# Kernel tuning notes

Measured on AMD Instinct MI355X. Metric: run time of the kernel, lower is better.

The kernel has to match this reference:

```python
import jax, jax.numpy as jnp
import numpy as np

B, S, D = 1, 2048, 1024
HEADS, HEAD_DIM = 16, 64
GRID = (8, 16, 16)      # frames, height, width; prod == S
WIN = (3, 5, 5)         # window_f, window_h, window_w
NEG = -1e9


def _window_mask_3d(frames, height, width, wf, wh, ww):
    """[S, S] bool mask: True where kv is inside the 3D local window of q."""
    idx = np.arange(frames * height * width)
    f = idx // (height * width)
    hw = idx % (height * width)
    h = hw // width
    w = hw % width
    mf = np.abs(f[:, None] - f[None, :]) <= wf // 2
    mh = np.abs(h[:, None] - h[None, :]) <= wh // 2
    mw = np.abs(w[:, None] - w[None, :]) <= ww // 2
    return jnp.asarray(mf & mh & mw)


def setup_inputs() -> dict:
    key = jax.random.key(0)
    ks = jax.random.split(key, 6)
    sd = 1.0 / np.sqrt(D)
    return {
        "hidden_states": jax.random.normal(ks[0], (B, S, D), jnp.float32),
        "Wq": jax.random.normal(ks[1], (D, D), jnp.float32) * sd,
        "Wk": jax.random.normal(ks[2], (D, D), jnp.float32) * sd,
        "Wv": jax.random.normal(ks[3], (D, D), jnp.float32) * sd,
        "Wo": jax.random.normal(ks[4], (D, D), jnp.float32) * sd,
        "bo": jnp.zeros((D,), jnp.float32),
        "frames": GRID[0], "height": GRID[1], "width": GRID[2],
        "wf": WIN[0], "wh": WIN[1], "ww": WIN[2],
    }


def reference(hidden_states, Wq, Wk, Wv, Wo, bo, frames, height, width, wf, wh, ww):
    b, s, d = hidden_states.shape
    hd = d // HEADS
    scale = 1.0 / np.sqrt(hd)

    # QKV projections (attn.to_q / to_k / to_v, bias=False), self-attention
    q = (hidden_states @ Wq).reshape(b, s, HEADS, hd).transpose(0, 2, 1, 3)
    k = (hidden_states @ Wk).reshape(b, s, HEADS, hd).transpose(0, 2, 1, 3)
    v = (hidden_states @ Wv).reshape(b, s, HEADS, hd).transpose(0, 2, 1, 3)

    mask = _window_mask_3d(frames, height, width, wf, wh, ww)  # [S, S] bool

    # SDPA with boolean attn_mask (window-based block-sparse pattern)
    scores = jnp.einsum("bhqd,bhkd->bhqk", q, k) * scale
    scores = jnp.where(mask[None, None], scores, NEG)
    attnw = jax.nn.softmax(scores, axis=-1)
    out = jnp.einsum("bhqk,bhkd->bhqd", attnw, v)

    out = out.transpose(0, 2, 1, 3).reshape(b, s, d)
    return out @ Wo + bo
```

## Files before the change

### kernel.cpp

```cpp
#include <hip/hip_runtime.h>
#include <hip/hip_bf16.h>
#include <hip/hip_fp16.h>

#define SEQ   2048
#define DIM   1024
#define NHEAD 16
#define HD    64
#define QSCALE 0.18033688011112042f

typedef _Float16 half8 __attribute__((ext_vector_type(8)));
typedef _Float16 half4 __attribute__((ext_vector_type(4)));
typedef float    floatx4 __attribute__((ext_vector_type(4)));

__device__ __forceinline__ void gload16(const void* g, void* l) {
    __builtin_amdgcn_global_load_lds(
        (const __attribute__((address_space(1))) unsigned int*)g,
        (__attribute__((address_space(3))) unsigned int*)l, 16, 0, 0);
}

#define VMCNT(n) asm volatile("s_waitcnt vmcnt(" #n ")" ::: "memory")
#define LGKM0()  asm volatile("s_waitcnt lgkmcnt(0)" ::: "memory")
#define BAR()    __builtin_amdgcn_s_barrier()

__global__ __launch_bounds__(256) void prep(
        const float* __restrict__ H, _Float16* __restrict__ Hf,
        const float* __restrict__ W0, const float* __restrict__ W1,
        const float* __restrict__ W2, const float* __restrict__ W3,
        _Float16* __restrict__ T) {
    __shared__ float tile[64][65];
    int z = blockIdx.z;
    int t = threadIdx.x;
    if (z < 4) {
        const float* W = (z == 0) ? W0 : (z == 1) ? W1 : (z == 2) ? W2 : W3;
        _Float16* Tz = T + (size_t)z * (DIM * DIM);
        int bx = blockIdx.x * 64;
        int by = blockIdx.y * 64;
        #pragma unroll
        for (int i = 0; i < 4; i++) {
            int id = t + i * 256;
            int r = id >> 4;
            int c = (id & 15) * 4;
            float4 v = *reinterpret_cast<const float4*>(W + (size_t)(by + r) * DIM + bx + c);
            tile[r][c] = v.x; tile[r][c + 1] = v.y; tile[r][c + 2] = v.z; tile[r][c + 3] = v.w;
        }
        __syncthreads();
        #pragma unroll
        for (int i = 0; i < 2; i++) {
            int id = t + i * 256;
            int nr = id >> 3;
            int c8 = id & 7;
            half8 o;
            #pragma unroll
            for (int j = 0; j < 8; j++) o[j] = (_Float16)tile[c8 * 8 + j][nr];
            *reinterpret_cast<half8*>(Tz + (size_t)(bx + nr) * DIM + by + c8 * 8) = o;
        }
    } else {
        int wg = blockIdx.y * 16 + blockIdx.x;
        #pragma unroll
        for (int i = 0; i < 4; i++) {
            int base = ((wg * 4 + i) * 256 + t) * 8;
            float4 v0 = *reinterpret_cast<const float4*>(H + base);
            float4 v1 = *reinterpret_cast<const float4*>(H + base + 4);
            half8 o = { (_Float16)v0.x, (_Float16)v0.y, (_Float16)v0.z, (_Float16)v0.w,
                        (_Float16)v1.x, (_Float16)v1.y, (_Float16)v1.z, (_Float16)v1.w };
            *reinterpret_cast<half8*>(Hf + base) = o;
        }
    }
}

__device__ __forceinline__ void gemm_core(const _Float16* __restrict__ Ap,
                                          const _Float16* __restrict__ Bp,
                                          char* lds, floatx4 (&acc)[4][4]) {
    const int tid  = threadIdx.x;
    const int lane = tid & 63;
    const int wid  = tid >> 6;
    const int wr = wid >> 1, wc = wid & 1;
    const int r16 = lane & 15;
    const int kk  = (lane >> 4) * 8;

    const int srow = tid >> 2, scol = (tid & 3) * 8;
    const _Float16* As0 = Ap + (size_t)srow * DIM + scol;
    const _Float16* Bs0 = Bp + (size_t)srow * DIM + scol;

    auto stage = [&](int buf, int t) {
        char* Ad = lds + buf * 32768;
        char* Bd = Ad + 16384;
        int k0 = t * 64;
        #pragma unroll
        for (int i = 0; i < 4; i++) {
            int off = (i & 1) * 64 * DIM + (i >> 1) * 32 + k0;
            gload16(As0 + off, Ad + i * 4096 + wid * 1024);
            gload16(Bs0 + off, Bd + i * 4096 + wid * 1024);
        }
    };

    auto compute = [&](int buf) {
        char* Ad = lds + buf * 32768;
        char* Bd = Ad + 16384;
        #pragma unroll
        for (int ks = 0; ks < 2; ks++) {
            half8 a[4], b[4];
            #pragma unroll
            for (int m = 0; m < 4; m++)
                a[m] = *reinterpret_cast<half8*>(Ad + ks * 8192 + (wr * 64 + m * 16 + r16) * 64 + kk * 2);
            #pragma unroll
            for (int n = 0; n < 4; n++)
                b[n] = *reinterpret_cast<half8*>(Bd + ks * 8192 + (wc * 64 + n * 16 + r16) * 64 + kk * 2);
            #pragma unroll
            for (int m = 0; m < 4; m++)
                #pragma unroll
                for (int n = 0; n < 4; n++)
                    acc[m][n] = __builtin_amdgcn_mfma_f32_16x16x32_f16(a[m], b[n], acc[m][n], 0, 0, 0);
        }
    };

    stage(0, 0);
    stage(1, 1);
    #pragma unroll 1
    for (int t = 0; t < 14; t += 2) {
        VMCNT(8); BAR();
        compute(0);
        BAR();
        stage(0, t + 2);
        VMCNT(8); BAR();
        compute(1);
        BAR();
        stage(1, t + 3);
    }
    VMCNT(8); BAR();
    compute(0);
    BAR();
    VMCNT(0); BAR();
    compute(1);
}

__device__ __forceinline__ void gemm_core64(const _Float16* __restrict__ Ap,
                                            const _Float16* __restrict__ Bp,
                                            char* lds, floatx4 (&acc)[4][2]) {
    const int tid  = threadIdx.x;
    const int lane = tid & 63;
    const int wid  = tid >> 6;
    const int wr = wid >> 1, wc = wid & 1;
    const int r16 = lane & 15;
    const int kk  = (lane >> 4) * 8;

    const int srow = tid >> 2, scol = (tid & 3) * 8;
    const _Float16* As0 = Ap + (size_t)srow * DIM + scol;
    const _Float16* Bs0 = Bp + (size_t)srow * DIM + scol;

    auto stage = [&](int buf, int t) {
        char* Ad = lds + buf * 24576;
        char* Bd = Ad + 16384;
        int k0 = t * 64;
        #pragma unroll
        for (int i = 0; i < 4; i++) {
            int off = (i & 1) * 64 * DIM + (i >> 1) * 32 + k0;
            gload16(As0 + off, Ad + i * 4096 + wid * 1024);
        }
        #pragma unroll
        for (int j = 0; j < 2; j++)
            gload16(Bs0 + j * 32 + k0, Bd + j * 4096 + wid * 1024);
    };

    auto compute = [&](int buf) {
        char* Ad = lds + buf * 24576;
        char* Bd = Ad + 16384;
        #pragma unroll
        for (int ks = 0; ks < 2; ks++) {
            half8 a[4], b[2];
            #pragma unroll
            for (int m = 0; m < 4; m++)
                a[m] = *reinterpret_cast<half8*>(Ad + ks * 8192 + (wr * 64 + m * 16 + r16) * 64 + kk * 2);
            #pragma unroll
            for (int n = 0; n < 2; n++)
                b[n] = *reinterpret_cast<half8*>(Bd + ks * 4096 + (wc * 32 + n * 16 + r16) * 64 + kk * 2);
            #pragma unroll
            for (int m = 0; m < 4; m++)
                #pragma unroll
                for (int n = 0; n < 2; n++)
                    acc[m][n] = __builtin_amdgcn_mfma_f32_16x16x32_f16(a[m], b[n], acc[m][n], 0, 0, 0);
        }
    };

    stage(0, 0);
    stage(1, 1);
    #pragma unroll 1
    for (int t = 0; t < 14; t += 2) {
        VMCNT(6); BAR();
        compute(0);
        BAR();
        stage(0, t + 2);
        VMCNT(6); BAR();
        compute(1);
        BAR();
        stage(1, t + 3);
    }
    VMCNT(6); BAR();
    compute(0);
    BAR();
    VMCNT(0); BAR();
    compute(1);
}

__global__ __launch_bounds__(256) void gemm_qkv(
        const _Float16* __restrict__ Hf, const _Float16* __restrict__ Wt,
        _Float16* __restrict__ Qp, _Float16* __restrict__ Kp, _Float16* __restrict__ Vt) {
    __shared__ char lds[65536];
    floatx4 acc[4][4] = {};

    int lin = blockIdx.x + 16 * blockIdx.y + 128 * blockIdx.z;
    int swz = (lin & 7) * 48 + (lin >> 3);
    int z  = swz >> 7;
    int rem = swz & 127;
    int bx = rem & 15, by = rem >> 4;

    int tm, tn;
    const _Float16 *Ap, *Bp;
    if (z < 2) {
        tm = bx; tn = by;
        Ap = Hf + (size_t)tm * 128 * DIM;
        Bp = Wt + (size_t)z * DIM * DIM + (size_t)tn * 128 * DIM;
    } else {
        tm = bx & 7; tn = by * 2 + (bx >> 3);
        Ap = Wt + (size_t)2 * DIM * DIM + (size_t)tm * 128 * DIM;
        Bp = Hf + (size_t)tn * 128 * DIM;
    }
    gemm_core(Ap, Bp, lds, acc);

    int lane = threadIdx.x & 63, wid = threadIdx.x >> 6;
    int wr = wid >> 1, wc = wid & 1;
    float qs = (z == 0) ? QSCALE : 1.0f;
    _Float16* Oz = (z == 0) ? Qp : Kp;

    #pragma unroll
    for (int m = 0; m < 4; m++) {
        #pragma unroll
        for (int n = 0; n < 4; n++) {
            #pragma unroll
            for (int r = 0; r < 4; r++) {
                int row = tm * 128 + wr * 64 + m * 16 + (lane >> 4) * 4 + r;
                int col = tn * 128 + wc * 64 + n * 16 + (lane & 15);
                float v = acc[m][n][r];
                if (z < 2) {
                    int head = col >> 6;
                    Oz[(size_t)head * (SEQ * HD) + (size_t)row * HD + (col & 63)] = (_Float16)(v * qs);
                } else {
                    Vt[(size_t)row * SEQ + col] = (_Float16)v;
                }
            }
        }
    }
}

__global__ __launch_bounds__(256) void gemm_o(
        const _Float16* __restrict__ AO, const _Float16* __restrict__ WoT,
        const float* __restrict__ bias, float* __restrict__ out) {
    __shared__ char lds[49152];
    floatx4 acc[4][2] = {};

    int lin = blockIdx.x + 16 * blockIdx.y;
    int swz = (lin & 7) * 32 + (lin >> 3);
    int tm = swz & 15, tn = swz >> 4;

    gemm_core64(AO + (size_t)tm * 128 * DIM, WoT + (size_t)tn * 64 * DIM, lds, acc);

    int lane = threadIdx.x & 63, wid = threadIdx.x >> 6;
    int wr = wid >> 1, wc = wid & 1;
    #pragma unroll
    for (int m = 0; m < 4; m++) {
        #pragma unroll
        for (int n = 0; n < 2; n++) {
            #pragma unroll
            for (int r = 0; r < 4; r++) {
                int row = tm * 128 + wr * 64 + m * 16 + (lane >> 4) * 4 + r;
                int col = tn * 64 + wc * 32 + n * 16 + (lane & 15);
                out[(size_t)row * DIM + col] = acc[m][n][r] + bias[col];
            }
        }
    }
}

__global__ __launch_bounds__(256) void attn_mfma(
        const _Float16* __restrict__ Q,
        const _Float16* __restrict__ K,
        const _Float16* __restrict__ Vt,
        _Float16* __restrict__ AO) {
    __shared__ char P_lds[4][16 * 640];

    int wid  = threadIdx.x >> 6;
    int lane = threadIdx.x & 63;
    int g    = lane >> 4;
    int ql   = lane & 15;

    int blk  = blockIdx.x;
    int sblk = (blk & 7) * 64 + (blk >> 3);
    int bid  = sblk * 4 + wid;
    int rid  = bid & 127;
    int head = bid >> 7;
    int f    = rid >> 4;
    int hq   = rid & 15;
    int s0   = rid << 4;

    const _Float16* Qh = Q  + (size_t)head * (SEQ * HD);
    const _Float16* Kh = K  + (size_t)head * (SEQ * HD);
    const _Float16* Vh = Vt + (size_t)head * (HD * SEQ);

    int f_start = min(max(f - 1, 0), 5);
    int h_start = min(max(hq - 2, 0), 10);

    bool wm[4];
    #pragma unroll
    for (int r = 0; r < 4; r++) {
        int wp = g * 4 + r;
        wm[r] = (wp - ql <= 2) && (ql - wp <= 2);
    }

    half8 qf[2];
    #pragma unroll
    for (int ks = 0; ks < 2; ks++)
        qf[ks] = *reinterpret_cast<const half8*>(Qh + (size_t)(s0 + ql) * HD + ks * 32 + g * 8);

    float lsum = 0.f;
    int swz = (ql & 7) << 4;

    #pragma unroll
    for (int fi = 0; fi < 3; fi++) {
        int fp = f_start + fi;
        bool fok = (fp - f <= 1) && (f - fp <= 1);
        int sbase = fp * 256 + h_start * 16;
        const _Float16* Kc = Kh + (size_t)sbase * HD;

        floatx4 sacc[6];
        #pragma unroll
        for (int j = 0; j < 6; j++) sacc[j] = (floatx4){0.f, 0.f, 0.f, 0.f};

        __builtin_amdgcn_s_setprio(1);
        #pragma unroll
        for (int j = 0; j < 6; j++) {
            #pragma unroll
            for (int ks = 0; ks < 2; ks++) {
                half8 kf = *reinterpret_cast<const half8*>(Kc + (size_t)(j * 16 + ql) * HD + ks * 32 + g * 8);
                sacc[j] = __builtin_amdgcn_mfma_f32_16x16x32_f16(kf, qf[ks], sacc[j], 0, 0, 0);
            }
        }
        __builtin_amdgcn_s_setprio(0);

        #pragma unroll
        for (int j = 0; j < 6; j++) {
            int hp = h_start + j;
            bool ok = fok && (hp - hq <= 2) && (hq - hp <= 2);
            half4 pv;
            #pragma unroll
            for (int r = 0; r < 4; r++) {
                float sv = (ok && wm[r]) ? sacc[j][r] : -10000.f;
                float p  = __builtin_amdgcn_exp2f(sv);
                lsum += p;
                pv[r] = (_Float16)p;
            }
            int byte = (ql * 640 + (fi * 96 + j * 16 + g * 4) * 2) ^ swz;
            *reinterpret_cast<half4*>(&P_lds[wid][byte]) = pv;
        }
    }

    lsum += __shfl_xor(lsum, 16);
    lsum += __shfl_xor(lsum, 32);
    float inv = __builtin_amdgcn_rcpf(lsum);

    LGKM0();

    floatx4 oacc[4];
    #pragma unroll
    for (int dt = 0; dt < 4; dt++) oacc[dt] = (floatx4){0.f, 0.f, 0.f, 0.f};

    #pragma unroll
    for (int fi = 0; fi < 3; fi++) {
        int sbase = (f_start + fi) * 256 + h_start * 16;
        __builtin_amdgcn_s_setprio(1);
        #pragma unroll
        for (int kw = 0; kw < 3; kw++) {
            int kcol = fi * 96 + kw * 32;
            int byte = (ql * 640 + (kcol + g * 8) * 2) ^ swz;
            half8 pa = *reinterpret_cast<half8*>(&P_lds[wid][byte]);
            #pragma unroll
            for (int dt = 0; dt < 4; dt++) {
                half8 vf = *reinterpret_cast<const half8*>(
                    Vh + (size_t)(dt * 16 + ql) * SEQ + sbase + kw * 32 + g * 8);
                oacc[dt] = __builtin_amdgcn_mfma_f32_16x16x32_f16(pa, vf, oacc[dt], 0, 0, 0);
            }
        }
        __builtin_amdgcn_s_setprio(0);
    }

    #pragma unroll
    for (int rr = 0; rr < 4; rr++) {
        float invr = __shfl(inv, g * 4 + rr);
        #pragma unroll
        for (int dt = 0; dt < 4; dt++) {
            AO[(size_t)(s0 + g * 4 + rr) * DIM + head * HD + dt * 16 + ql] =
                (_Float16)(oacc[dt][rr] * invr);
        }
    }
}

extern "C" void kernel_launch(void* const* d_in, const int* in_sizes, int n_in,
                              void* d_out, int out_size, void* d_ws, size_t ws_size,
                              hipStream_t stream) {
    const float* H  = (const float*)d_in[0];
    const float* Wq = (const float*)d_in[1];
    const float* Wk = (const float*)d_in[2];
    const float* Wv = (const float*)d_in[3];
    const float* Wo = (const float*)d_in[4];
    const float* bo = (const float*)d_in[5];

    char* ws = (char*)d_ws;
    _Float16* Hf = (_Float16*)(ws);
    _Float16* Wt = (_Float16*)(ws + (4u  << 20));
    _Float16* Qp = (_Float16*)(ws + (12u << 20));
    _Float16* Kp = (_Float16*)(ws + (16u << 20));
    _Float16* Vt = (_Float16*)(ws + (20u << 20));
    _Float16* AO = (_Float16*)(ws + (24u << 20));

    prep<<<dim3(16, 16, 5), 256, 0, stream>>>(H, Hf, Wq, Wk, Wv, Wo, Wt);

    gemm_qkv<<<dim3(16, 8, 3), 256, 0, stream>>>(Hf, Wt, Qp, Kp, Vt);

    attn_mfma<<<dim3(NHEAD * 128 / 4), 256, 0, stream>>>(Qp, Kp, Vt, AO);

    gemm_o<<<dim3(16, 16), 256, 0, stream>>>(AO, Wt + (size_t)3 * DIM * DIM, bo, (float*)d_out);
}
```

Before: 59.97 us.

## Fuse Q and K projections per head tile sharing A loads, split V into 128x64 tiles

The QKV projection kernel is restructured so each Q/K workgroup computes one head's Q and K output together (128 rows by 64 columns each), loading the hidden-state tile once and reusing it for both weight matrices. V uses the narrower 128x64 gemm_core64 path. The grid grows from 384 to 512 workgroups, which should fill the CUs better and cut redundant A-tile traffic. The trade-off is smaller per-matrix N tiles, which lowers arithmetic intensity on the B side.

Result: slower. 61.18 us (+2.0%).

```diff
diff --git a/kernel.cpp b/kernel.cpp
--- a/kernel.cpp
+++ b/kernel.cpp
@@ -68,72 +68,6 @@
     }
 }
 
-__device__ __forceinline__ void gemm_core(const _Float16* __restrict__ Ap,
-                                          const _Float16* __restrict__ Bp,
-                                          char* lds, floatx4 (&acc)[4][4]) {
-    const int tid  = threadIdx.x;
-    const int lane = tid & 63;
-    const int wid  = tid >> 6;
-    const int wr = wid >> 1, wc = wid & 1;
-    const int r16 = lane & 15;
-    const int kk  = (lane >> 4) * 8;
-
-    const int srow = tid >> 2, scol = (tid & 3) * 8;
-    const _Float16* As0 = Ap + (size_t)srow * DIM + scol;
-    const _Float16* Bs0 = Bp + (size_t)srow * DIM + scol;
-
-    auto stage = [&](int buf, int t) {
-        char* Ad = lds + buf * 32768;
-        char* Bd = Ad + 16384;
-        int k0 = t * 64;
-        #pragma unroll
-        for (int i = 0; i < 4; i++) {
-            int off = (i & 1) * 64 * DIM + (i >> 1) * 32 + k0;
-            gload16(As0 + off, Ad + i * 4096 + wid * 1024);
-            gload16(Bs0 + off, Bd + i * 4096 + wid * 1024);
-        }
-    };
-
-    auto compute = [&](int buf) {
-        char* Ad = lds + buf * 32768;
-        char* Bd = Ad + 16384;
-        #pragma unroll
-        for (int ks = 0; ks < 2; ks++) {
-            half8 a[4], b[4];
-            #pragma unroll
-            for (int m = 0; m < 4; m++)
-                a[m] = *reinterpret_cast<half8*>(Ad + ks * 8192 + (wr * 64 + m * 16 + r16) * 64 + kk * 2);
-            #pragma unroll
-            for (int n = 0; n < 4; n++)
-                b[n] = *reinterpret_cast<half8*>(Bd + ks * 8192 + (wc * 64 + n * 16 + r16) * 64 + kk * 2);
-            #pragma unroll
-            for (int m = 0; m < 4; m++)
-                #pragma unroll
-                for (int n = 0; n < 4; n++)
-                    acc[m][n] = __builtin_amdgcn_mfma_f32_16x16x32_f16(a[m], b[n], acc[m][n], 0, 0, 0);
-        }
-    };
-
-    stage(0, 0);
-    stage(1, 1);
-    #pragma unroll 1
-    for (int t = 0; t < 14; t += 2) {
-        VMCNT(8); BAR();
-        compute(0);
-        BAR();
-        stage(0, t + 2);
-        VMCNT(8); BAR();
-        compute(1);
-        BAR();
-        stage(1, t + 3);
-    }
-    VMCNT(8); BAR();
-    compute(0);
-    BAR();
-    VMCNT(0); BAR();
-    compute(1);
-}
-
 __device__ __forceinline__ void gemm_core64(const _Float16* __restrict__ Ap,
                                             const _Float16* __restrict__ Bp,
                                             char* lds, floatx4 (&acc)[4][2]) {
@@ -206,46 +140,111 @@
         const _Float16* __restrict__ Hf, const _Float16* __restrict__ Wt,
         _Float16* __restrict__ Qp, _Float16* __restrict__ Kp, _Float16* __restrict__ Vt) {
     __shared__ char lds[65536];
-    floatx4 acc[4][4] = {};
-
-    int lin = blockIdx.x + 16 * blockIdx.y + 128 * blockIdx.z;
-    int swz = (lin & 7) * 48 + (lin >> 3);
-    int z  = swz >> 7;
-    int rem = swz & 127;
-    int bx = rem & 15, by = rem >> 4;
-
-    int tm, tn;
-    const _Float16 *Ap, *Bp;
-    if (z < 2) {
-        tm = bx; tn = by;
-        Ap = Hf + (size_t)tm * 128 * DIM;
-        Bp = Wt + (size_t)z * DIM * DIM + (size_t)tn * 128 * DIM;
+
+    int lin = blockIdx.x + 256 * blockIdx.z;
+    int swz = (lin & 7) * 64 + (lin >> 3);
+    int z   = swz >> 8;
+    int rem = swz & 255;
+
+    const int tid  = threadIdx.x;
+    const int lane = tid & 63;
+    const int wid  = tid >> 6;
+    const int wr = wid >> 1, wc = wid & 1;
+    const int r16 = lane & 15;
+    const int kk  = (lane >> 4) * 8;
+    const int srow = tid >> 2, scol = (tid & 3) * 8;
+
+    if (z == 0) {
+        int tm = rem & 15, tn = rem >> 4;
+        const _Float16* As0 = Hf + (size_t)tm * 128 * DIM + (size_t)srow * DIM + scol;
+        const _Float16* Bq0 = Wt + (size_t)tn * 64 * DIM + (size_t)srow * DIM + scol;
+        const _Float16* Bk0 = Wt + (size_t)DIM * DIM + (size_t)tn * 64 * DIM + (size_t)srow * DIM + scol;
+        floatx4 accQ[4][2] = {}, accK[4][2] = {};
+
+        auto stage = [&](int buf, int t) {
+            char* Ad = lds + buf * 32768;
+            int k0 = t * 64;
+            #pragma unroll
+            for (int i = 0; i < 4; i++) {
+                int off = (i & 1) * 64 * DIM + (i >> 1) * 32 + k0;
+                gload16(As0 + off, Ad + i * 4096 + wid * 1024);
+            }
+            #pragma unroll
+            for (int j = 0; j < 2; j++) {
+                gload16(Bq0 + j * 32 + k0, Ad + 16384 + j * 4096 + wid * 1024);
+                gload16(Bk0 + j * 32 + k0, Ad + 24576 + j * 4096 + wid * 1024);
+            }
+        };
+        auto compute = [&](int buf) {
+            char* Ad = lds + buf * 32768;
+            #pragma unroll
+            for (int ks = 0; ks < 2; ks++) {
+                half8 a[4], bq[2], bk[2];
+                #pragma unroll
+                for (int m = 0; m < 4; m++)
+                    a[m] = *reinterpret_cast<half8*>(Ad + ks * 8192 + (wr * 64 + m * 16 + r16) * 64 + kk * 2);
+                #pragma unroll
+                for (int n = 0; n < 2; n++) {
+                    bq[n] = *reinterpret_cast<half8*>(Ad + 16384 + ks * 4096 + (wc * 32 + n * 16 + r16) * 64 + kk * 2);
+                    bk[n] = *reinterpret_cast<half8*>(Ad + 24576 + ks * 4096 + (wc * 32 + n * 16 + r16) * 64 + kk * 2);
+                }
+                #pragma unroll
+                for (int m = 0; m < 4; m++)
+                    #pragma unroll
+                    for (int n = 0; n < 2; n++) {
+                        accQ[m][n] = __builtin_amdgcn_mfma_f32_16x16x32_f16(a[m], bq[n], accQ[m][n], 0, 0, 0);
+                        accK[m][n] = __builtin_amdgcn_mfma_f32_16x16x32_f16(a[m], bk[n], accK[m][n], 0, 0, 0);
+                    }
+            }
+        };
+
+        stage(0, 0);
+        stage(1, 1);
+        #pragma unroll 1
+        for (int t = 0; t < 14; t += 2) {
+            VMCNT(8); BAR();
+            compute(0);
+            BAR();
+            stage(0, t + 2);
+            VMCNT(8); BAR();
+            compute(1);
+            BAR();
+            stage(1, t + 3);
+        }
+        VMCNT(8); BAR();
+        compute(0);
+        BAR();
+        VMCNT(0); BAR();
+        compute(1);
+
+        #pragma unroll
+        for (int m = 0; m < 4; m++) {
+            #pragma unroll
+            for (int n = 0; n < 2; n++) {
+                #pragma unroll
+                for (int r = 0; r < 4; r++) {
+                    int row = tm * 128 + wr * 64 + m * 16 + (lane >> 4) * 4 + r;
+                    int col = wc * 32 + n * 16 + r16;
+                    size_t off = (size_t)tn * (SEQ * HD) + (size_t)row * HD + col;
+                    Qp[off] = (_Float16)(accQ[m][n][r] * QSCALE);
+                    Kp[off] = (_Float16)accK[m][n][r];
+                }
+            }
+        }
     } else {
-        tm = bx & 7; tn = by * 2 + (bx >> 3);
-        Ap = Wt + (size_t)2 * DIM * DIM + (size_t)tm * 128 * DIM;
-        Bp = Hf + (size_t)tn * 128 * DIM;
-    }
-    gemm_core(Ap, Bp, lds, acc);
-
-    int lane = threadIdx.x & 63, wid = threadIdx.x >> 6;
-    int wr = wid >> 1, wc = wid & 1;
-    float qs = (z == 0) ? QSCALE : 1.0f;
-    _Float16* Oz = (z == 0) ? Qp : Kp;
-
-    #pragma unroll
-    for (int m = 0; m < 4; m++) {
-        #pragma unroll
-        for (int n = 0; n < 4; n++) {
-            #pragma unroll
-            for (int r = 0; r < 4; r++) {
-                int row = tm * 128 + wr * 64 + m * 16 + (lane >> 4) * 4 + r;
-                int col = tn * 128 + wc * 64 + n * 16 + (lane & 15);
-                float v = acc[m][n][r];
-                if (z < 2) {
-                    int head = col >> 6;
-                    Oz[(size_t)head * (SEQ * HD) + (size_t)row * HD + (col & 63)] = (_Float16)(v * qs);
-                } else {
-                    Vt[(size_t)row * SEQ + col] = (_Float16)v;
+        int tm = rem & 7, tn = rem >> 3;
+        floatx4 acc[4][2] = {};
+        gemm_core64(Wt + (size_t)2 * DIM * DIM + (size_t)tm * 128 * DIM,
+                    Hf + (size_t)tn * 64 * DIM, lds, acc);
+        #pragma unroll
+        for (int m = 0; m < 4; m++) {
+            #pragma unroll
+            for (int n = 0; n < 2; n++) {
+                #pragma unroll
+                for (int r = 0; r < 4; r++) {
+                    int row = tm * 128 + wr * 64 + m * 16 + (lane >> 4) * 4 + r;
+                    int col = tn * 64 + wc * 32 + n * 16 + r16;
+                    Vt[(size_t)row * SEQ + col] = (_Float16)acc[m][n][r];
                 }
             }
         }
@@ -422,7 +421,7 @@
 
     prep<<<dim3(16, 16, 5), 256, 0, stream>>>(H, Hf, Wq, Wk, Wv, Wo, Wt);
 
-    gemm_qkv<<<dim3(16, 8, 3), 256, 0, stream>>>(Hf, Wt, Qp, Kp, Vt);
+    gemm_qkv<<<dim3(256, 1, 2), 256, 0, stream>>>(Hf, Wt, Qp, Kp, Vt);
 
     attn_mfma<<<dim3(NHEAD * 128 / 4), 256, 0, stream>>>(Qp, Kp, Vt, AO);
 
```
